# Kernel tuning notes

Hardware: AMD Instinct MI355X
Metric: run time of the kernel (lower is better)

Reference implementation:

```python
import jax, jax.numpy as jnp
import numpy as np

N_NODES = 20000
N_EDGES = 100000
WIDTH = 64
KER_IN = 6
KER_HID = WIDTH // 4  # 16
DEPTH = 6


def setup_inputs() -> dict:
    key = jax.random.key(0)
    ks = jax.random.split(key, 12)
    s = lambda fan_in: 1.0 / np.sqrt(fan_in)
    return {
        "x": jax.random.normal(ks[0], (N_NODES, 1), dtype=jnp.float32),
        "edge_index": jax.random.randint(ks[1], (2, N_EDGES), 0, N_NODES, dtype=jnp.int32),
        "edge_attr": jax.random.uniform(ks[2], (N_EDGES, KER_IN), dtype=jnp.float32),
        "fc1_w": jax.random.normal(ks[3], (1, WIDTH), dtype=jnp.float32) * s(1),
        "fc1_b": jnp.zeros((WIDTH,), dtype=jnp.float32),
        "k1_w": jax.random.normal(ks[4], (KER_IN, KER_HID), dtype=jnp.float32) * s(KER_IN),
        "k1_b": jnp.zeros((KER_HID,), dtype=jnp.float32),
        "k2_w": jax.random.normal(ks[5], (KER_HID, WIDTH * WIDTH), dtype=jnp.float32) * s(KER_HID),
        "k2_b": jnp.zeros((WIDTH * WIDTH,), dtype=jnp.float32),
        "root_w": jax.random.normal(ks[6], (WIDTH, WIDTH), dtype=jnp.float32) * s(WIDTH),
        "conv_b": jnp.zeros((WIDTH,), dtype=jnp.float32),
        "fc2_w": jax.random.normal(ks[7], (WIDTH, 1), dtype=jnp.float32) * s(WIDTH),
        "fc2_b": jnp.zeros((1,), dtype=jnp.float32),
    }


def reference(x, edge_index, edge_attr, fc1_w, fc1_b, k1_w, k1_b, k2_w, k2_b,
              root_w, conv_b, fc2_w, fc2_b):
    src = edge_index[0]  # source nodes j
    dst = edge_index[1]  # target nodes i

    # fc1: lift node features [N,1] -> [N,W]
    h = x @ fc1_w + fc1_b

    # Edge-conditioned weight matrices via kernel MLP (edge_attr is layer-invariant,
    # so compute once and reuse for all DEPTH layers — identical math).
    ek = jax.nn.relu(edge_attr @ k1_w + k1_b)           # [E, W/4]
    W = (ek @ k2_w + k2_b).reshape(N_EDGES, WIDTH, WIDTH)  # [E, W, W]

    # mean aggregation denominator (in-degree, clamped to avoid div-by-zero)
    deg = jax.ops.segment_sum(jnp.ones((N_EDGES,), dtype=h.dtype), dst,
                              num_segments=N_NODES)
    denom = jnp.maximum(deg, 1.0)[:, None]               # [N,1]

    for _ in range(DEPTH):
        # per-edge matmul: msg_e = x_src[e] @ W_e
        msg = jnp.einsum('ei,eio->eo', h[src], W)        # [E, W]
        agg = jax.ops.segment_sum(msg, dst, num_segments=N_NODES) / denom
        h = jax.nn.relu(agg + h @ root_w + conv_b)       # NNConv root weight + bias, then outer ReLU

    return h @ fc2_w + fc2_b                              # [N, 1]
```

## Files before the change

### kernel.cpp

```cpp
#include <hip/hip_runtime.h>
#include <hip/hip_bf16.h>


#define NN 20000
#define NE 100000
#define WD 64
#define DEPTH 6
#define TM 15
#define LSTR 1092

typedef __attribute__((ext_vector_type(8))) short bf16x8;
typedef __attribute__((ext_vector_type(4))) float f32x4;

__device__ __forceinline__ unsigned short f2bf(float v) {
    union { float f; unsigned u; } x; x.f = v;
    unsigned r = x.u + 0x7fffu + ((x.u >> 16) & 1u);
    return (unsigned short)(r >> 16);
}
__device__ __forceinline__ float bf2f(unsigned short b) {
    union { unsigned u; float f; } x; x.u = ((unsigned)b) << 16;
    return x.f;
}

__global__ __launch_bounds__(256) void count_kernel(const int* __restrict__ ei,
                                                    int* __restrict__ outc,
                                                    int* __restrict__ inc)
{
    int e = blockIdx.x * 256 + threadIdx.x;
    if (e >= NE) return;
    atomicAdd(&outc[ei[e]], 1);
    atomicAdd(&inc[ei[NE + e]], 1);
}

__global__ __launch_bounds__(256) void scanA_kernel(const int* __restrict__ cnt,
                                                    int* __restrict__ partials)
{
    int b = blockIdx.x, t = threadIdx.x, lane = t & 63, w = t >> 6;
    int base = b * 1024 + t * 4;
    int s = 0;
#pragma unroll
    for (int i = 0; i < 4; ++i) {
        int idx = base + i;
        if (idx < 2 * NN) s += cnt[idx];
    }
#pragma unroll
    for (int off = 32; off > 0; off >>= 1) s += __shfl_down(s, off, 64);
    __shared__ int wsum[4];
    if (lane == 0) wsum[w] = s;
    __syncthreads();
    if (t == 0) partials[b] = wsum[0] + wsum[1] + wsum[2] + wsum[3];
}

__global__ __launch_bounds__(64) void scanB_kernel(const int* __restrict__ partials,
                                                   int* __restrict__ bases)
{
    int l = threadIdx.x;
    int p = (l < 40) ? partials[l] : 0;
    int v = p;
#pragma unroll
    for (int off = 1; off < 64; off <<= 1) {
        int u = __shfl_up(v, off, 64);
        if (l >= off) v += u;
    }
    if (l < 40) bases[l] = v - p;
}

__global__ __launch_bounds__(256) void scanC_kernel(const int* __restrict__ cnt,
                                                    const int* __restrict__ bases,
                                                    int* __restrict__ rps,
                                                    int* __restrict__ rpd,
                                                    float* __restrict__ invd)
{
    int b = blockIdx.x, t = threadIdx.x, lane = t & 63, w = t >> 6;
    int base = b * 1024 + t * 4;
    int v[4], s = 0;
#pragma unroll
    for (int i = 0; i < 4; ++i) {
        int idx = base + i;
        v[i] = (idx < 2 * NN) ? cnt[idx] : 0;
        s += v[i];
    }
    int tsum = s, sc = s;
#pragma unroll
    for (int off = 1; off < 64; off <<= 1) {
        int u = __shfl_up(sc, off, 64);
        if (lane >= off) sc += u;
    }
    __shared__ int wtot[4];
    if (lane == 63) wtot[w] = sc;
    __syncthreads();
    int wbase = 0;
    for (int j = 0; j < w; ++j) wbase += wtot[j];
    int run = bases[b] + wbase + sc - tsum;
#pragma unroll
    for (int i = 0; i < 4; ++i) {
        int idx = base + i;
        int e = run; run += v[i];
        if (idx < NN) {
            rps[idx] = e;
        } else if (idx < 2 * NN) {
            rpd[idx - NN] = e - NE;
            invd[idx - NN] = 1.0f / fmaxf((float)v[i], 1.0f);
        }
    }
    if (b == 0 && t == 0) { rps[NN] = NE; rpd[NN] = NE; }
}

__global__ __launch_bounds__(256) void ekfill_kernel(
    const int* __restrict__ ei, const float* __restrict__ ea,
    const float* __restrict__ k1w, const float* __restrict__ k1b,
    const int* __restrict__ rps, const int* __restrict__ rpd,
    int* __restrict__ fs, int* __restrict__ fd,
    float* __restrict__ eks, int* __restrict__ ss2sd)
{
    int e = blockIdx.x * 256 + threadIdx.x;
    if (e >= NE) return;
    int s = ei[e], d = ei[NE + e];
    float a[6];
#pragma unroll
    for (int i = 0; i < 6; ++i) a[i] = ea[e * 6 + i];
    int slot_s = rps[s] + atomicAdd(&fs[s], 1);
    int slot_d = rpd[d] + atomicAdd(&fd[d], 1);
    ss2sd[slot_s] = slot_d;
#pragma unroll
    for (int j = 0; j < 16; ++j) {
        float v = k1b[j];
#pragma unroll
        for (int i = 0; i < 6; ++i) v = fmaf(a[i], k1w[i * 16 + j], v);
        eks[(size_t)slot_s * 16 + j] = fmaxf(v, 0.f);
    }
}

__global__ __launch_bounds__(256) void gwt_kernel(
    const float* __restrict__ k2w, const float* __restrict__ k2b,
    const float* __restrict__ rootw,
    unsigned short* __restrict__ Gh, unsigned short* __restrict__ Gl)
{
    int idx = blockIdx.x * 256 + threadIdx.x;
    if (idx >= 1152 * 64) return;
    int n = idx >> 6, k = idx & 63;
    int b = n >> 6, o = n & 63;
    float g;
    if (b < 16)       g = k2w[b * 4096 + k * 64 + o];
    else if (b == 16) g = k2b[k * 64 + o];
    else              g = rootw[k * 64 + o];
    unsigned short hi = f2bf(g);
    Gh[idx] = hi;
    Gl[idx] = f2bf(g - bf2f(hi));
}

__global__ __launch_bounds__(256) void h0_kernel(
    const float* __restrict__ x, const float* __restrict__ w,
    const float* __restrict__ b,
    unsigned short* __restrict__ hhi, unsigned short* __restrict__ hlo)
{
    int idx = blockIdx.x * 256 + threadIdx.x;
    if (idx >= NN * WD) return;
    int n = idx >> 6, o = idx & 63;
    float v = fmaf(x[n], w[o], b[o]);
    unsigned short hi = f2bf(v);
    hhi[idx] = hi;
    hlo[idx] = f2bf(v - bf2f(hi));
}

__global__ __launch_bounds__(512) void fused_kernel(
    const unsigned short* __restrict__ hhi, const unsigned short* __restrict__ hlo,
    const unsigned short* __restrict__ Gh, const unsigned short* __restrict__ Gl,
    const float* __restrict__ eks, const int* __restrict__ ss2sd,
    const int* __restrict__ rps, float* __restrict__ Proot,
    float* __restrict__ msg)
{
    __shared__ __align__(16) float Pt[TM * LSTR];
    __shared__ int rb[TM + 1];
    int n0 = blockIdx.x * TM;
    int w = threadIdx.x >> 6, l = threadIdx.x & 63;
    int quad = l >> 4, lr = l & 15;
    if (threadIdx.x < TM + 1) {
        int gi = n0 + threadIdx.x;
        rb[threadIdx.x] = rps[gi > NN ? NN : gi];
    }
    int arow = n0 + lr;
    if (arow > NN - 1) arow = NN - 1;
    const bf16x8* pah = (const bf16x8*)(hhi + (size_t)arow * 64 + quad * 8);
    const bf16x8* pal = (const bf16x8*)(hlo + (size_t)arow * 64 + quad * 8);
    bf16x8 ah0 = pah[0], ah1 = pah[4];
    bf16x8 al0 = pal[0], al1 = pal[4];

    for (int st = w; st < 18; st += 8) {
        f32x4 acc[4];
#pragma unroll
        for (int t = 0; t < 4; ++t) acc[t] = (f32x4){0.f, 0.f, 0.f, 0.f};
#pragma unroll
        for (int t = 0; t < 4; ++t) {
            int brow = st * 64 + t * 16 + lr;
            const bf16x8* pbh = (const bf16x8*)(Gh + (size_t)brow * 64 + quad * 8);
            const bf16x8* pbl = (const bf16x8*)(Gl + (size_t)brow * 64 + quad * 8);
            bf16x8 bh0 = pbh[0], bh1 = pbh[4];
            bf16x8 bl0 = pbl[0], bl1 = pbl[4];
            f32x4 a = acc[t];
            a = __builtin_amdgcn_mfma_f32_16x16x32_bf16(ah0, bh0, a, 0, 0, 0);
            a = __builtin_amdgcn_mfma_f32_16x16x32_bf16(ah0, bl0, a, 0, 0, 0);
            a = __builtin_amdgcn_mfma_f32_16x16x32_bf16(al0, bh0, a, 0, 0, 0);
            a = __builtin_amdgcn_mfma_f32_16x16x32_bf16(ah1, bh1, a, 0, 0, 0);
            a = __builtin_amdgcn_mfma_f32_16x16x32_bf16(ah1, bl1, a, 0, 0, 0);
            a = __builtin_amdgcn_mfma_f32_16x16x32_bf16(al1, bh1, a, 0, 0, 0);
            acc[t] = a;
        }
        if (st < 17) {
#pragma unroll
            for (int t = 0; t < 4; ++t)
#pragma unroll
                for (int r = 0; r < 4; ++r) {
                    int row = quad * 4 + r;
                    if (row < TM)
                        Pt[row * LSTR + st * 64 + t * 16 + lr] = acc[t][r];
                }
        } else {
#pragma unroll
            for (int t = 0; t < 4; ++t)
#pragma unroll
                for (int r = 0; r < 4; ++r) {
                    int row = quad * 4 + r;
                    int gn = n0 + row;
                    if (row < TM && gn < NN)
                        Proot[(size_t)gn * 64 + t * 16 + lr] = acc[t][r];
                }
        }
    }
    __syncthreads();

    int nend = n0 + TM; if (nend > NN) nend = NN;
    int r0 = rb[0], r1 = rb[nend - n0];
    int total = r1 - r0;
    if (total <= 0) return;
    int per = (total + 7) >> 3;
    int s0 = r0 + w * per;
    int s1 = s0 + per; if (s1 > r1) s1 = r1;
    int ln = 0;
    float p[17];
    bool need = true;
    for (int s = s0; s < s1; ++s) {
        while (s >= rb[ln + 1]) { ++ln; need = true; }
        if (need) {
            const float* Pr = &Pt[ln * LSTR];
#pragma unroll
            for (int k = 0; k < 17; ++k) p[k] = Pr[k * 64 + l];
            need = false;
        }
        int su = __builtin_amdgcn_readfirstlane(s);
        const float* er = eks + (size_t)su * 16;
        f32x4 e0 = *(const f32x4*)(er);
        f32x4 e1 = *(const f32x4*)(er + 4);
        f32x4 e2 = *(const f32x4*)(er + 8);
        f32x4 e3 = *(const f32x4*)(er + 12);
        int ds = ss2sd[su];
        float ma = p[16], mb = 0.f;
        ma = fmaf(e0[0], p[0], ma);  mb = fmaf(e0[1], p[1], mb);
        ma = fmaf(e0[2], p[2], ma);  mb = fmaf(e0[3], p[3], mb);
        ma = fmaf(e1[0], p[4], ma);  mb = fmaf(e1[1], p[5], mb);
        ma = fmaf(e1[2], p[6], ma);  mb = fmaf(e1[3], p[7], mb);
        ma = fmaf(e2[0], p[8], ma);  mb = fmaf(e2[1], p[9], mb);
        ma = fmaf(e2[2], p[10], ma); mb = fmaf(e2[3], p[11], mb);
        ma = fmaf(e3[0], p[12], ma); mb = fmaf(e3[1], p[13], mb);
        ma = fmaf(e3[2], p[14], ma); mb = fmaf(e3[3], p[15], mb);
        msg[(size_t)ds * 64 + l] = ma + mb;
    }
}

__global__ __launch_bounds__(256) void agg_kernel(
    const float* __restrict__ msg, const int* __restrict__ rpd,
    const float* __restrict__ invd, const float* __restrict__ Proot,
    const float* __restrict__ convb, float* __restrict__ h,
    unsigned short* __restrict__ hhi, unsigned short* __restrict__ hlo)
{
    int i = blockIdx.x * 4 + (threadIdx.x >> 6);
    if (i >= NN) return;
    int l = threadIdx.x & 63;
    int r0 = rpd[i], r1 = rpd[i + 1];
    float a0 = 0.f, a1 = 0.f, a2 = 0.f, a3 = 0.f;
    int s = r0;
    for (; s + 3 < r1; s += 4) {
        a0 += msg[(size_t)s * 64 + l];
        a1 += msg[(size_t)(s + 1) * 64 + l];
        a2 += msg[(size_t)(s + 2) * 64 + l];
        a3 += msg[(size_t)(s + 3) * 64 + l];
    }
    for (; s < r1; ++s) a0 += msg[(size_t)s * 64 + l];
    float acc = (a0 + a1) + (a2 + a3);
    float v = fmaf(acc, invd[i], Proot[(size_t)i * 64 + l] + convb[l]);
    v = fmaxf(v, 0.f);
    int idx = i * 64 + l;
    h[idx] = v;
    unsigned short hi = f2bf(v);
    hhi[idx] = hi;
    hlo[idx] = f2bf(v - bf2f(hi));
}

__global__ __launch_bounds__(256) void out_kernel(
    const float* __restrict__ h, const float* __restrict__ fc2_w,
    const float* __restrict__ fc2_b, float* __restrict__ out)
{
    int wave = blockIdx.x * 4 + (threadIdx.x >> 6);
    int lane = threadIdx.x & 63;
    float v = h[(size_t)wave * 64 + lane] * fc2_w[lane];
#pragma unroll
    for (int off = 32; off > 0; off >>= 1) v += __shfl_down(v, off);
    if (lane == 0) out[wave] = v + fc2_b[0];
}

extern "C" void kernel_launch(void* const* d_in, const int* in_sizes, int n_in,
                              void* d_out, int out_size, void* d_ws, size_t ws_size,
                              hipStream_t stream)
{
    const float* x         = (const float*)d_in[0];
    const int*   ei        = (const int*)  d_in[1];
    const float* edge_attr = (const float*)d_in[2];
    const float* fc1_w     = (const float*)d_in[3];
    const float* fc1_b     = (const float*)d_in[4];
    const float* k1_w      = (const float*)d_in[5];
    const float* k1_b      = (const float*)d_in[6];
    const float* k2_w      = (const float*)d_in[7];
    const float* k2_b      = (const float*)d_in[8];
    const float* root_w    = (const float*)d_in[9];
    const float* conv_b    = (const float*)d_in[10];
    const float* fc2_w     = (const float*)d_in[11];
    const float* fc2_b     = (const float*)d_in[12];
    float* out = (float*)d_out;

    float* ws = (float*)d_ws;
    size_t off = 0;
    int* cnt   = (int*)(ws + off); off += 4 * NN;
    int* outc  = cnt;
    int* inc   = cnt + NN;
    int* fs    = cnt + 2 * NN;
    int* fd    = cnt + 3 * NN;
    int* rps   = (int*)(ws + off); off += 20004;
    int* rpd   = (int*)(ws + off); off += 20004;
    int* partials = (int*)(ws + off); off += 64;
    int* bases    = (int*)(ws + off); off += 64;
    int* ss2sd    = (int*)(ws + off); off += NE;
    float* invd  = ws + off; off += NN;
    float* eks   = ws + off; off += (size_t)NE * 16;
    unsigned short* Gh  = (unsigned short*)(ws + off); off += 36864;
    unsigned short* Gl  = (unsigned short*)(ws + off); off += 36864;
    unsigned short* hhi = (unsigned short*)(ws + off); off += (size_t)NN * 32;
    unsigned short* hlo = (unsigned short*)(ws + off); off += (size_t)NN * 32;
    float* h     = ws + off; off += (size_t)NN * WD;
    float* msg   = ws + off; off += (size_t)NE * WD;
    float* Proot = ws + off; off += (size_t)NN * WD;

    hipMemsetAsync(cnt, 0, 4 * NN * sizeof(int), stream);
    count_kernel<<<(NE + 255) / 256, 256, 0, stream>>>(ei, outc, inc);
    scanA_kernel<<<40, 256, 0, stream>>>(cnt, partials);
    scanB_kernel<<<1, 64, 0, stream>>>(partials, bases);
    scanC_kernel<<<40, 256, 0, stream>>>(cnt, bases, rps, rpd, invd);
    ekfill_kernel<<<(NE + 255) / 256, 256, 0, stream>>>(ei, edge_attr, k1_w, k1_b,
                                                        rps, rpd, fs, fd, eks, ss2sd);
    gwt_kernel<<<(1152 * 64 + 255) / 256, 256, 0, stream>>>(k2_w, k2_b, root_w, Gh, Gl);
    h0_kernel<<<(NN * WD + 255) / 256, 256, 0, stream>>>(x, fc1_w, fc1_b, hhi, hlo);

    int ntiles = (NN + TM - 1) / TM;
    for (int layer = 0; layer < DEPTH; ++layer) {
        fused_kernel<<<ntiles, 512, 0, stream>>>(hhi, hlo, Gh, Gl, eks, ss2sd,
                                                 rps, Proot, msg);
        agg_kernel<<<(NN + 3) / 4, 256, 0, stream>>>(msg, rpd, invd, Proot,
                                                     conv_b, h, hhi, hlo);
    }

    out_kernel<<<NN / 4, 256, 0, stream>>>(h, fc2_w, fc2_b, out);
}
```

Before: 561.8 us.

## Aggregate per-destination edge features before the weight matmul, fusing layers into one kernel

The per-layer pipeline is reordered. Each destination node's incoming edges are first reduced into a 17x64 accumulator, z[k] = sum of ek[k]*h_src plus a plain h_src sum for the bias term, built in shared memory with LDS atomics. One bf16x3 MFMA against the transposed k2/k2b weights then produces the mean-aggregated message, and the root matmul, bias, ReLU and bf16 split are fused into the same kernel. This removes the per-edge msg buffer, the separate aggregation kernel and the source-side CSR, and ping-pongs the h buffers between layers. In exchange it adds a scalar gather of h rows per edge, LDS atomics, and a per-tile conversion of z to bf16 hi/lo pairs.

```diff
diff --git a/kernel.cpp b/kernel.cpp
--- a/kernel.cpp
+++ b/kernel.cpp
@@ -7,7 +7,7 @@
 #define WD 64
 #define DEPTH 6
 #define TM 15
-#define LSTR 1092
+#define ZSTR 1092
 
 typedef __attribute__((ext_vector_type(8))) short bf16x8;
 typedef __attribute__((ext_vector_type(4))) float f32x4;
@@ -23,12 +23,10 @@
 }
 
 __global__ __launch_bounds__(256) void count_kernel(const int* __restrict__ ei,
-                                                    int* __restrict__ outc,
                                                     int* __restrict__ inc)
 {
     int e = blockIdx.x * 256 + threadIdx.x;
     if (e >= NE) return;
-    atomicAdd(&outc[ei[e]], 1);
     atomicAdd(&inc[ei[NE + e]], 1);
 }
 
@@ -41,7 +39,7 @@
 #pragma unroll
     for (int i = 0; i < 4; ++i) {
         int idx = base + i;
-        if (idx < 2 * NN) s += cnt[idx];
+        if (idx < NN) s += cnt[idx];
     }
 #pragma unroll
     for (int off = 32; off > 0; off >>= 1) s += __shfl_down(s, off, 64);
@@ -55,19 +53,18 @@
                                                    int* __restrict__ bases)
 {
     int l = threadIdx.x;
-    int p = (l < 40) ? partials[l] : 0;
+    int p = (l < 20) ? partials[l] : 0;
     int v = p;
 #pragma unroll
     for (int off = 1; off < 64; off <<= 1) {
         int u = __shfl_up(v, off, 64);
         if (l >= off) v += u;
     }
-    if (l < 40) bases[l] = v - p;
+    if (l < 20) bases[l] = v - p;
 }
 
 __global__ __launch_bounds__(256) void scanC_kernel(const int* __restrict__ cnt,
                                                     const int* __restrict__ bases,
-                                                    int* __restrict__ rps,
                                                     int* __restrict__ rpd,
                                                     float* __restrict__ invd)
 {
@@ -77,7 +74,7 @@
 #pragma unroll
     for (int i = 0; i < 4; ++i) {
         int idx = base + i;
-        v[i] = (idx < 2 * NN) ? cnt[idx] : 0;
+        v[i] = (idx < NN) ? cnt[idx] : 0;
         s += v[i];
     }
     int tsum = s, sc = s;
@@ -97,21 +94,18 @@
         int idx = base + i;
         int e = run; run += v[i];
         if (idx < NN) {
-            rps[idx] = e;
-        } else if (idx < 2 * NN) {
-            rpd[idx - NN] = e - NE;
-            invd[idx - NN] = 1.0f / fmaxf((float)v[i], 1.0f);
-        }
-    }
-    if (b == 0 && t == 0) { rps[NN] = NE; rpd[NN] = NE; }
+            rpd[idx] = e;
+            invd[idx] = 1.0f / fmaxf((float)v[i], 1.0f);
+        }
+    }
+    if (b == 0 && t == 0) rpd[NN] = NE;
 }
 
 __global__ __launch_bounds__(256) void ekfill_kernel(
     const int* __restrict__ ei, const float* __restrict__ ea,
     const float* __restrict__ k1w, const float* __restrict__ k1b,
-    const int* __restrict__ rps, const int* __restrict__ rpd,
-    int* __restrict__ fs, int* __restrict__ fd,
-    float* __restrict__ eks, int* __restrict__ ss2sd)
+    const int* __restrict__ rpd, int* __restrict__ fd,
+    float* __restrict__ eks, int* __restrict__ srcs)
 {
     int e = blockIdx.x * 256 + threadIdx.x;
     if (e >= NE) return;
@@ -119,15 +113,14 @@
     float a[6];
 #pragma unroll
     for (int i = 0; i < 6; ++i) a[i] = ea[e * 6 + i];
-    int slot_s = rps[s] + atomicAdd(&fs[s], 1);
-    int slot_d = rpd[d] + atomicAdd(&fd[d], 1);
-    ss2sd[slot_s] = slot_d;
+    int slot = rpd[d] + atomicAdd(&fd[d], 1);
+    srcs[slot] = s;
 #pragma unroll
     for (int j = 0; j < 16; ++j) {
         float v = k1b[j];
 #pragma unroll
         for (int i = 0; i < 6; ++i) v = fmaf(a[i], k1w[i * 16 + j], v);
-        eks[(size_t)slot_s * 16 + j] = fmaxf(v, 0.f);
+        eks[(size_t)slot * 16 + j] = fmaxf(v, 0.f);
     }
 }
 
@@ -137,13 +130,12 @@
     unsigned short* __restrict__ Gh, unsigned short* __restrict__ Gl)
 {
     int idx = blockIdx.x * 256 + threadIdx.x;
-    if (idx >= 1152 * 64) return;
-    int n = idx >> 6, k = idx & 63;
-    int b = n >> 6, o = n & 63;
+    if (idx >= 64 * 1152) return;
+    int o = idx / 1152, c = idx % 1152;
     float g;
-    if (b < 16)       g = k2w[b * 4096 + k * 64 + o];
-    else if (b == 16) g = k2b[k * 64 + o];
-    else              g = rootw[k * 64 + o];
+    if (c < 1024)       g = k2w[(c >> 6) * 4096 + (c & 63) * 64 + o];
+    else if (c < 1088)  g = k2b[(c & 63) * 64 + o];
+    else                g = rootw[(c - 1088) * 64 + o];
     unsigned short hi = f2bf(g);
     Gh[idx] = hi;
     Gl[idx] = f2bf(g - bf2f(hi));
@@ -151,149 +143,161 @@
 
 __global__ __launch_bounds__(256) void h0_kernel(
     const float* __restrict__ x, const float* __restrict__ w,
-    const float* __restrict__ b,
+    const float* __restrict__ b, float* __restrict__ h,
     unsigned short* __restrict__ hhi, unsigned short* __restrict__ hlo)
 {
     int idx = blockIdx.x * 256 + threadIdx.x;
     if (idx >= NN * WD) return;
     int n = idx >> 6, o = idx & 63;
     float v = fmaf(x[n], w[o], b[o]);
-    unsigned short hi = f2bf(v);
-    hhi[idx] = hi;
-    hlo[idx] = f2bf(v - bf2f(hi));
-}
-
-__global__ __launch_bounds__(512) void fused_kernel(
-    const unsigned short* __restrict__ hhi, const unsigned short* __restrict__ hlo,
-    const unsigned short* __restrict__ Gh, const unsigned short* __restrict__ Gl,
-    const float* __restrict__ eks, const int* __restrict__ ss2sd,
-    const int* __restrict__ rps, float* __restrict__ Proot,
-    float* __restrict__ msg)
-{
-    __shared__ __align__(16) float Pt[TM * LSTR];
-    __shared__ int rb[TM + 1];
-    int n0 = blockIdx.x * TM;
-    int w = threadIdx.x >> 6, l = threadIdx.x & 63;
-    int quad = l >> 4, lr = l & 15;
-    if (threadIdx.x < TM + 1) {
-        int gi = n0 + threadIdx.x;
-        rb[threadIdx.x] = rps[gi > NN ? NN : gi];
-    }
-    int arow = n0 + lr;
-    if (arow > NN - 1) arow = NN - 1;
-    const bf16x8* pah = (const bf16x8*)(hhi + (size_t)arow * 64 + quad * 8);
-    const bf16x8* pal = (const bf16x8*)(hlo + (size_t)arow * 64 + quad * 8);
-    bf16x8 ah0 = pah[0], ah1 = pah[4];
-    bf16x8 al0 = pal[0], al1 = pal[4];
-
-    for (int st = w; st < 18; st += 8) {
-        f32x4 acc[4];
-#pragma unroll
-        for (int t = 0; t < 4; ++t) acc[t] = (f32x4){0.f, 0.f, 0.f, 0.f};
-#pragma unroll
-        for (int t = 0; t < 4; ++t) {
-            int brow = st * 64 + t * 16 + lr;
-            const bf16x8* pbh = (const bf16x8*)(Gh + (size_t)brow * 64 + quad * 8);
-            const bf16x8* pbl = (const bf16x8*)(Gl + (size_t)brow * 64 + quad * 8);
-            bf16x8 bh0 = pbh[0], bh1 = pbh[4];
-            bf16x8 bl0 = pbl[0], bl1 = pbl[4];
-            f32x4 a = acc[t];
-            a = __builtin_amdgcn_mfma_f32_16x16x32_bf16(ah0, bh0, a, 0, 0, 0);
-            a = __builtin_amdgcn_mfma_f32_16x16x32_bf16(ah0, bl0, a, 0, 0, 0);
-            a = __builtin_amdgcn_mfma_f32_16x16x32_bf16(al0, bh0, a, 0, 0, 0);
-            a = __builtin_amdgcn_mfma_f32_16x16x32_bf16(ah1, bh1, a, 0, 0, 0);
-            a = __builtin_amdgcn_mfma_f32_16x16x32_bf16(ah1, bl1, a, 0, 0, 0);
-            a = __builtin_amdgcn_mfma_f32_16x16x32_bf16(al1, bh1, a, 0, 0, 0);
-            acc[t] = a;
-        }
-        if (st < 17) {
-#pragma unroll
-            for (int t = 0; t < 4; ++t)
-#pragma unroll
-                for (int r = 0; r < 4; ++r) {
-                    int row = quad * 4 + r;
-                    if (row < TM)
-                        Pt[row * LSTR + st * 64 + t * 16 + lr] = acc[t][r];
-                }
-        } else {
-#pragma unroll
-            for (int t = 0; t < 4; ++t)
-#pragma unroll
-                for (int r = 0; r < 4; ++r) {
-                    int row = quad * 4 + r;
-                    int gn = n0 + row;
-                    if (row < TM && gn < NN)
-                        Proot[(size_t)gn * 64 + t * 16 + lr] = acc[t][r];
-                }
-        }
-    }
-    __syncthreads();
-
-    int nend = n0 + TM; if (nend > NN) nend = NN;
-    int r0 = rb[0], r1 = rb[nend - n0];
-    int total = r1 - r0;
-    if (total <= 0) return;
-    int per = (total + 7) >> 3;
-    int s0 = r0 + w * per;
-    int s1 = s0 + per; if (s1 > r1) s1 = r1;
-    int ln = 0;
-    float p[17];
-    bool need = true;
-    for (int s = s0; s < s1; ++s) {
-        while (s >= rb[ln + 1]) { ++ln; need = true; }
-        if (need) {
-            const float* Pr = &Pt[ln * LSTR];
-#pragma unroll
-            for (int k = 0; k < 17; ++k) p[k] = Pr[k * 64 + l];
-            need = false;
-        }
-        int su = __builtin_amdgcn_readfirstlane(s);
-        const float* er = eks + (size_t)su * 16;
-        f32x4 e0 = *(const f32x4*)(er);
-        f32x4 e1 = *(const f32x4*)(er + 4);
-        f32x4 e2 = *(const f32x4*)(er + 8);
-        f32x4 e3 = *(const f32x4*)(er + 12);
-        int ds = ss2sd[su];
-        float ma = p[16], mb = 0.f;
-        ma = fmaf(e0[0], p[0], ma);  mb = fmaf(e0[1], p[1], mb);
-        ma = fmaf(e0[2], p[2], ma);  mb = fmaf(e0[3], p[3], mb);
-        ma = fmaf(e1[0], p[4], ma);  mb = fmaf(e1[1], p[5], mb);
-        ma = fmaf(e1[2], p[6], ma);  mb = fmaf(e1[3], p[7], mb);
-        ma = fmaf(e2[0], p[8], ma);  mb = fmaf(e2[1], p[9], mb);
-        ma = fmaf(e2[2], p[10], ma); mb = fmaf(e2[3], p[11], mb);
-        ma = fmaf(e3[0], p[12], ma); mb = fmaf(e3[1], p[13], mb);
-        ma = fmaf(e3[2], p[14], ma); mb = fmaf(e3[3], p[15], mb);
-        msg[(size_t)ds * 64 + l] = ma + mb;
-    }
-}
-
-__global__ __launch_bounds__(256) void agg_kernel(
-    const float* __restrict__ msg, const int* __restrict__ rpd,
-    const float* __restrict__ invd, const float* __restrict__ Proot,
-    const float* __restrict__ convb, float* __restrict__ h,
-    unsigned short* __restrict__ hhi, unsigned short* __restrict__ hlo)
-{
-    int i = blockIdx.x * 4 + (threadIdx.x >> 6);
-    if (i >= NN) return;
-    int l = threadIdx.x & 63;
-    int r0 = rpd[i], r1 = rpd[i + 1];
-    float a0 = 0.f, a1 = 0.f, a2 = 0.f, a3 = 0.f;
-    int s = r0;
-    for (; s + 3 < r1; s += 4) {
-        a0 += msg[(size_t)s * 64 + l];
-        a1 += msg[(size_t)(s + 1) * 64 + l];
-        a2 += msg[(size_t)(s + 2) * 64 + l];
-        a3 += msg[(size_t)(s + 3) * 64 + l];
-    }
-    for (; s < r1; ++s) a0 += msg[(size_t)s * 64 + l];
-    float acc = (a0 + a1) + (a2 + a3);
-    float v = fmaf(acc, invd[i], Proot[(size_t)i * 64 + l] + convb[l]);
-    v = fmaxf(v, 0.f);
-    int idx = i * 64 + l;
     h[idx] = v;
     unsigned short hi = f2bf(v);
     hhi[idx] = hi;
     hlo[idx] = f2bf(v - bf2f(hi));
+}
+
+__global__ __launch_bounds__(512) void fused2_kernel(
+    const float* __restrict__ h, const unsigned short* __restrict__ hhi,
+    const unsigned short* __restrict__ hlo,
+    const unsigned short* __restrict__ Gh, const unsigned short* __restrict__ Gl,
+    const float* __restrict__ eks, const int* __restrict__ srcs,
+    const int* __restrict__ rpd, const float* __restrict__ invd,
+    const float* __restrict__ convb, float* __restrict__ hout,
+    unsigned short* __restrict__ hhio, unsigned short* __restrict__ hloo)
+{
+    __shared__ __align__(16) float Zt[TM * ZSTR];
+    __shared__ int rb[TM + 1];
+    int n0 = blockIdx.x * TM;
+    int tid = threadIdx.x;
+    int w = tid >> 6, l = tid & 63;
+    int quad = l >> 4, lr = l & 15;
+    if (tid < TM + 1) {
+        int gi = n0 + tid;
+        rb[tid] = rpd[gi > NN ? NN : gi];
+    }
+    for (int i = tid; i < TM * ZSTR; i += 512) Zt[i] = 0.f;
+    __syncthreads();
+
+    int nend = n0 + TM; if (nend > NN) nend = NN;
+    int tmeff = nend - n0;
+    int r0 = rb[0], r1 = rb[tmeff];
+    int total = r1 - r0;
+    if (total > 0) {
+        int per = (total + 7) >> 3;
+        int s0 = r0 + w * per;
+        int s1 = s0 + per; if (s1 > r1) s1 = r1;
+        if (s0 < s1) {
+            int ln = 0;
+            while (s0 >= rb[ln + 1]) ++ln;
+            float z[17];
+#pragma unroll
+            for (int k = 0; k < 17; ++k) z[k] = 0.f;
+            bool dirty = false;
+            for (int s = s0; s < s1; ++s) {
+                if (s >= rb[ln + 1]) {
+                    if (dirty) {
+#pragma unroll
+                        for (int k = 0; k < 17; ++k)
+                            atomicAdd(&Zt[ln * ZSTR + k * 64 + l], z[k]);
+#pragma unroll
+                        for (int k = 0; k < 17; ++k) z[k] = 0.f;
+                        dirty = false;
+                    }
+                    while (s >= rb[ln + 1]) ++ln;
+                }
+                int su = __builtin_amdgcn_readfirstlane(s);
+                int sn = srcs[su];
+                float hv = h[(size_t)sn * 64 + l];
+                const float* er = eks + (size_t)su * 16;
+                f32x4 e0 = *(const f32x4*)(er);
+                f32x4 e1 = *(const f32x4*)(er + 4);
+                f32x4 e2 = *(const f32x4*)(er + 8);
+                f32x4 e3 = *(const f32x4*)(er + 12);
+                z[0]  = fmaf(e0[0], hv, z[0]);   z[1]  = fmaf(e0[1], hv, z[1]);
+                z[2]  = fmaf(e0[2], hv, z[2]);   z[3]  = fmaf(e0[3], hv, z[3]);
+                z[4]  = fmaf(e1[0], hv, z[4]);   z[5]  = fmaf(e1[1], hv, z[5]);
+                z[6]  = fmaf(e1[2], hv, z[6]);   z[7]  = fmaf(e1[3], hv, z[7]);
+                z[8]  = fmaf(e2[0], hv, z[8]);   z[9]  = fmaf(e2[1], hv, z[9]);
+                z[10] = fmaf(e2[2], hv, z[10]);  z[11] = fmaf(e2[3], hv, z[11]);
+                z[12] = fmaf(e3[0], hv, z[12]);  z[13] = fmaf(e3[1], hv, z[13]);
+                z[14] = fmaf(e3[2], hv, z[14]);  z[15] = fmaf(e3[3], hv, z[15]);
+                z[16] += hv;
+                dirty = true;
+            }
+            if (dirty) {
+#pragma unroll
+                for (int k = 0; k < 17; ++k)
+                    atomicAdd(&Zt[ln * ZSTR + k * 64 + l], z[k]);
+            }
+        }
+    }
+    __syncthreads();
+
+    int st = w & 3, kh = w >> 2;
+    int brow = st * 16 + lr;
+    int rowA = (lr < tmeff) ? lr : 0;
+    f32x4 acc = (f32x4){0.f, 0.f, 0.f, 0.f};
+    for (int ks = kh * 17; ks < kh * 17 + 17; ++ks) {
+        const f32x4* pz = (const f32x4*)&Zt[rowA * ZSTR + ks * 32 + quad * 8];
+        f32x4 z0 = pz[0], z1 = pz[1];
+        bf16x8 ah, al;
+#pragma unroll
+        for (int j = 0; j < 4; ++j) {
+            unsigned short hi0 = f2bf(z0[j]);
+            ah[j] = (short)hi0; al[j] = (short)f2bf(z0[j] - bf2f(hi0));
+            unsigned short hi1 = f2bf(z1[j]);
+            ah[4 + j] = (short)hi1; al[4 + j] = (short)f2bf(z1[j] - bf2f(hi1));
+        }
+        const bf16x8* pbh = (const bf16x8*)(Gh + (size_t)brow * 1152 + ks * 32 + quad * 8);
+        const bf16x8* pbl = (const bf16x8*)(Gl + (size_t)brow * 1152 + ks * 32 + quad * 8);
+        bf16x8 bh = pbh[0], bl = pbl[0];
+        acc = __builtin_amdgcn_mfma_f32_16x16x32_bf16(ah, bh, acc, 0, 0, 0);
+        acc = __builtin_amdgcn_mfma_f32_16x16x32_bf16(ah, bl, acc, 0, 0, 0);
+        acc = __builtin_amdgcn_mfma_f32_16x16x32_bf16(al, bh, acc, 0, 0, 0);
+    }
+    f32x4 accR = (f32x4){0.f, 0.f, 0.f, 0.f};
+    if (kh == 1) {
+        int arow = n0 + lr;
+        if (arow > NN - 1) arow = NN - 1;
+#pragma unroll
+        for (int ks2 = 0; ks2 < 2; ++ks2) {
+            const bf16x8* pah = (const bf16x8*)(hhi + (size_t)arow * 64 + ks2 * 32 + quad * 8);
+            const bf16x8* pal = (const bf16x8*)(hlo + (size_t)arow * 64 + ks2 * 32 + quad * 8);
+            bf16x8 ah = pah[0], al = pal[0];
+            const bf16x8* pbh = (const bf16x8*)(Gh + (size_t)brow * 1152 + 1088 + ks2 * 32 + quad * 8);
+            const bf16x8* pbl = (const bf16x8*)(Gl + (size_t)brow * 1152 + 1088 + ks2 * 32 + quad * 8);
+            bf16x8 bh = pbh[0], bl = pbl[0];
+            accR = __builtin_amdgcn_mfma_f32_16x16x32_bf16(ah, bh, accR, 0, 0, 0);
+            accR = __builtin_amdgcn_mfma_f32_16x16x32_bf16(ah, bl, accR, 0, 0, 0);
+            accR = __builtin_amdgcn_mfma_f32_16x16x32_bf16(al, bh, accR, 0, 0, 0);
+        }
+    }
+    __syncthreads();
+    if (kh == 0) {
+#pragma unroll
+        for (int r = 0; r < 4; ++r)
+            Zt[st * 256 + (quad * 4 + r) * 16 + lr] = acc[r];
+    }
+    __syncthreads();
+    if (kh == 1) {
+        int col = st * 16 + lr;
+        float cb = convb[col];
+#pragma unroll
+        for (int r = 0; r < 4; ++r) {
+            int row = quad * 4 + r;
+            int gn = n0 + row;
+            if (row < tmeff) {
+                float aggv = acc[r] + Zt[st * 256 + row * 16 + lr];
+                float v = fmaf(aggv, invd[gn], accR[r] + cb);
+                v = fmaxf(v, 0.f);
+                size_t idx = (size_t)gn * 64 + col;
+                hout[idx] = v;
+                unsigned short hi = f2bf(v);
+                hhio[idx] = hi;
+                hloo[idx] = f2bf(v - bf2f(hi));
+            }
+        }
+    }
 }
 
 __global__ __launch_bounds__(256) void out_kernel(
@@ -329,43 +333,45 @@
 
     float* ws = (float*)d_ws;
     size_t off = 0;
-    int* cnt   = (int*)(ws + off); off += 4 * NN;
-    int* outc  = cnt;
-    int* inc   = cnt + NN;
-    int* fs    = cnt + 2 * NN;
-    int* fd    = cnt + 3 * NN;
-    int* rps   = (int*)(ws + off); off += 20004;
+    int* cnt   = (int*)(ws + off); off += 2 * NN;
+    int* inc   = cnt;
+    int* fd    = cnt + NN;
     int* rpd   = (int*)(ws + off); off += 20004;
     int* partials = (int*)(ws + off); off += 64;
     int* bases    = (int*)(ws + off); off += 64;
-    int* ss2sd    = (int*)(ws + off); off += NE;
+    int* srcs  = (int*)(ws + off); off += NE;
     float* invd  = ws + off; off += NN;
     float* eks   = ws + off; off += (size_t)NE * 16;
     unsigned short* Gh  = (unsigned short*)(ws + off); off += 36864;
     unsigned short* Gl  = (unsigned short*)(ws + off); off += 36864;
-    unsigned short* hhi = (unsigned short*)(ws + off); off += (size_t)NN * 32;
-    unsigned short* hlo = (unsigned short*)(ws + off); off += (size_t)NN * 32;
-    float* h     = ws + off; off += (size_t)NN * WD;
-    float* msg   = ws + off; off += (size_t)NE * WD;
-    float* Proot = ws + off; off += (size_t)NN * WD;
-
-    hipMemsetAsync(cnt, 0, 4 * NN * sizeof(int), stream);
-    count_kernel<<<(NE + 255) / 256, 256, 0, stream>>>(ei, outc, inc);
-    scanA_kernel<<<40, 256, 0, stream>>>(cnt, partials);
+    unsigned short* hhiA = (unsigned short*)(ws + off); off += (size_t)NN * 32;
+    unsigned short* hloA = (unsigned short*)(ws + off); off += (size_t)NN * 32;
+    unsigned short* hhiB = (unsigned short*)(ws + off); off += (size_t)NN * 32;
+    unsigned short* hloB = (unsigned short*)(ws + off); off += (size_t)NN * 32;
+    float* hA    = ws + off; off += (size_t)NN * WD;
+    float* hB    = ws + off; off += (size_t)NN * WD;
+
+    hipMemsetAsync(cnt, 0, 2 * NN * sizeof(int), stream);
+    count_kernel<<<(NE + 255) / 256, 256, 0, stream>>>(ei, inc);
+    scanA_kernel<<<20, 256, 0, stream>>>(inc, partials);
     scanB_kernel<<<1, 64, 0, stream>>>(partials, bases);
-    scanC_kernel<<<40, 256, 0, stream>>>(cnt, bases, rps, rpd, invd);
+    scanC_kernel<<<20, 256, 0, stream>>>(inc, bases, rpd, invd);
     ekfill_kernel<<<(NE + 255) / 256, 256, 0, stream>>>(ei, edge_attr, k1_w, k1_b,
-                                                        rps, rpd, fs, fd, eks, ss2sd);
-    gwt_kernel<<<(1152 * 64 + 255) / 256, 256, 0, stream>>>(k2_w, k2_b, root_w, Gh, Gl);
-    h0_kernel<<<(NN * WD + 255) / 256, 256, 0, stream>>>(x, fc1_w, fc1_b, hhi, hlo);
+                                                        rpd, fd, eks, srcs);
+    gwt_kernel<<<(64 * 1152 + 255) / 256, 256, 0, stream>>>(k2_w, k2_b, root_w, Gh, Gl);
+    h0_kernel<<<(NN * WD + 255) / 256, 256, 0, stream>>>(x, fc1_w, fc1_b, hA, hhiA, hloA);
 
     int ntiles = (NN + TM - 1) / TM;
+    float* hin = hA;  unsigned short* hhi_i = hhiA; unsigned short* hlo_i = hloA;
+    float* hto = hB;  unsigned short* hhi_o = hhiB; unsigned short* hlo_o = hloB;
     for (int layer = 0; layer < DEPTH; ++layer) {
-        fused_kernel<<<ntiles, 512, 0, stream>>>(hhi, hlo, Gh, Gl, eks, ss2sd,
-                                                 rps, Proot, msg);
-        agg_kernel<<<(NN + 3) / 4, 256, 0, stream>>>(msg, rpd, invd, Proot,
-                                                     conv_b, h, hhi, hlo);
-    }
-
-    out_kernel<<<NN / 4, 256, 0, stream>>>(h, fc2_w, fc2_b, out);
-}
+        fused2_kernel<<<ntiles, 512, 0, stream>>>(hin, hhi_i, hlo_i, Gh, Gl,
+                                                  eks, srcs, rpd, invd, conv_b,
+                                                  hto, hhi_o, hlo_o);
+        float* tf = hin; hin = hto; hto = tf;
+        unsigned short* t1 = hhi_i; hhi_i = hhi_o; hhi_o = t1;
+        unsigned short* t2 = hlo_i; hlo_i = hlo_o; hlo_o = t2;
+    }
+
+    out_kernel<<<NN / 4, 256, 0, stream>>>(hin, fc2_w, fc2_b, out);
+}
```

After: 1.350 ms. +140.3%, slower.

## Shrink node tile to 8, bound occupancy, restructure per-node edge loop

Applied to the files above, without the earlier changes.

Reduces nodes per block from 15 to 8, which halves the LDS tile and doubles the grid size. It also asks the compiler to fit 8 blocks per CU through launch bounds. The MFMA loop now computes and stores one 16-column tile at a time instead of holding four accumulators, and the edge loop iterates per node over clipped ranges instead of scanning row boundaries inside the edge loop. The aim is lower register and LDS pressure for more occupancy. The cost is that half the MFMA rows are wasted, since 16-row tiles now carry only 8 nodes, and the shared-weight B operand is reloaded by twice as many blocks.

```diff
diff --git a/kernel.cpp b/kernel.cpp
--- a/kernel.cpp
+++ b/kernel.cpp
@@ -6,7 +6,7 @@
 #define NE 100000
 #define WD 64
 #define DEPTH 6
-#define TM 15
+#define TM 8
 #define LSTR 1092
 
 typedef __attribute__((ext_vector_type(8))) short bf16x8;
@@ -163,7 +163,7 @@
     hlo[idx] = f2bf(v - bf2f(hi));
 }
 
-__global__ __launch_bounds__(512) void fused_kernel(
+__global__ __launch_bounds__(512, 8) void fused_kernel(
     const unsigned short* __restrict__ hhi, const unsigned short* __restrict__ hlo,
     const unsigned short* __restrict__ Gh, const unsigned short* __restrict__ Gl,
     const float* __restrict__ eks, const int* __restrict__ ss2sd,
@@ -187,83 +187,81 @@
     bf16x8 al0 = pal[0], al1 = pal[4];
 
     for (int st = w; st < 18; st += 8) {
-        f32x4 acc[4];
-#pragma unroll
-        for (int t = 0; t < 4; ++t) acc[t] = (f32x4){0.f, 0.f, 0.f, 0.f};
 #pragma unroll
         for (int t = 0; t < 4; ++t) {
             int brow = st * 64 + t * 16 + lr;
-            const bf16x8* pbh = (const bf16x8*)(Gh + (size_t)brow * 64 + quad * 8);
-            const bf16x8* pbl = (const bf16x8*)(Gl + (size_t)brow * 64 + quad * 8);
-            bf16x8 bh0 = pbh[0], bh1 = pbh[4];
-            bf16x8 bl0 = pbl[0], bl1 = pbl[4];
-            f32x4 a = acc[t];
-            a = __builtin_amdgcn_mfma_f32_16x16x32_bf16(ah0, bh0, a, 0, 0, 0);
-            a = __builtin_amdgcn_mfma_f32_16x16x32_bf16(ah0, bl0, a, 0, 0, 0);
-            a = __builtin_amdgcn_mfma_f32_16x16x32_bf16(al0, bh0, a, 0, 0, 0);
-            a = __builtin_amdgcn_mfma_f32_16x16x32_bf16(ah1, bh1, a, 0, 0, 0);
-            a = __builtin_amdgcn_mfma_f32_16x16x32_bf16(ah1, bl1, a, 0, 0, 0);
-            a = __builtin_amdgcn_mfma_f32_16x16x32_bf16(al1, bh1, a, 0, 0, 0);
-            acc[t] = a;
-        }
-        if (st < 17) {
-#pragma unroll
-            for (int t = 0; t < 4; ++t)
+            f32x4 a = (f32x4){0.f, 0.f, 0.f, 0.f};
+            {
+                const bf16x8* pbh = (const bf16x8*)(Gh + (size_t)brow * 64 + quad * 8);
+                const bf16x8* pbl = (const bf16x8*)(Gl + (size_t)brow * 64 + quad * 8);
+                bf16x8 bh0 = pbh[0], bl0 = pbl[0];
+                a = __builtin_amdgcn_mfma_f32_16x16x32_bf16(ah0, bh0, a, 0, 0, 0);
+                a = __builtin_amdgcn_mfma_f32_16x16x32_bf16(ah0, bl0, a, 0, 0, 0);
+                a = __builtin_amdgcn_mfma_f32_16x16x32_bf16(al0, bh0, a, 0, 0, 0);
+            }
+            {
+                const bf16x8* pbh = (const bf16x8*)(Gh + (size_t)brow * 64 + 32 + quad * 8);
+                const bf16x8* pbl = (const bf16x8*)(Gl + (size_t)brow * 64 + 32 + quad * 8);
+                bf16x8 bh1 = pbh[0], bl1 = pbl[0];
+                a = __builtin_amdgcn_mfma_f32_16x16x32_bf16(ah1, bh1, a, 0, 0, 0);
+                a = __builtin_amdgcn_mfma_f32_16x16x32_bf16(ah1, bl1, a, 0, 0, 0);
+                a = __builtin_amdgcn_mfma_f32_16x16x32_bf16(al1, bh1, a, 0, 0, 0);
+            }
+            if (st < 17) {
 #pragma unroll
                 for (int r = 0; r < 4; ++r) {
                     int row = quad * 4 + r;
                     if (row < TM)
-                        Pt[row * LSTR + st * 64 + t * 16 + lr] = acc[t][r];
+                        Pt[row * LSTR + st * 64 + t * 16 + lr] = a[r];
                 }
-        } else {
-#pragma unroll
-            for (int t = 0; t < 4; ++t)
+            } else {
 #pragma unroll
                 for (int r = 0; r < 4; ++r) {
                     int row = quad * 4 + r;
                     int gn = n0 + row;
                     if (row < TM && gn < NN)
-                        Proot[(size_t)gn * 64 + t * 16 + lr] = acc[t][r];
+                        Proot[(size_t)gn * 64 + t * 16 + lr] = a[r];
                 }
+            }
         }
     }
     __syncthreads();
 
     int nend = n0 + TM; if (nend > NN) nend = NN;
-    int r0 = rb[0], r1 = rb[nend - n0];
+    int tmeff = nend - n0;
+    int r0 = rb[0], r1 = rb[tmeff];
     int total = r1 - r0;
     if (total <= 0) return;
     int per = (total + 7) >> 3;
     int s0 = r0 + w * per;
     int s1 = s0 + per; if (s1 > r1) s1 = r1;
-    int ln = 0;
-    float p[17];
-    bool need = true;
-    for (int s = s0; s < s1; ++s) {
-        while (s >= rb[ln + 1]) { ++ln; need = true; }
-        if (need) {
-            const float* Pr = &Pt[ln * LSTR];
-#pragma unroll
-            for (int k = 0; k < 17; ++k) p[k] = Pr[k * 64 + l];
-            need = false;
+    for (int ln = 0; ln < tmeff && s0 < s1; ++ln) {
+        int lo = s0 > rb[ln] ? s0 : rb[ln];
+        int hi = s1 < rb[ln + 1] ? s1 : rb[ln + 1];
+        if (lo >= hi) continue;
+        float p[17];
+        const float* Pr = &Pt[ln * LSTR];
+#pragma unroll
+        for (int k = 0; k < 17; ++k) p[k] = Pr[k * 64 + l];
+        for (int s = lo; s < hi; ++s) {
+            int su = __builtin_amdgcn_readfirstlane(s);
+            const float* er = eks + (size_t)su * 16;
+            f32x4 e0 = *(const f32x4*)(er);
+            f32x4 e1 = *(const f32x4*)(er + 4);
+            f32x4 e2 = *(const f32x4*)(er + 8);
+            f32x4 e3 = *(const f32x4*)(er + 12);
+            int ds = ss2sd[su];
+            float ma = p[16], mb = 0.f;
+            ma = fmaf(e0[0], p[0], ma);  mb = fmaf(e0[1], p[1], mb);
+            ma = fmaf(e0[2], p[2], ma);  mb = fmaf(e0[3], p[3], mb);
+            ma = fmaf(e1[0], p[4], ma);  mb = fmaf(e1[1], p[5], mb);
+            ma = fmaf(e1[2], p[6], ma);  mb = fmaf(e1[3], p[7], mb);
+            ma = fmaf(e2[0], p[8], ma);  mb = fmaf(e2[1], p[9], mb);
+            ma = fmaf(e2[2], p[10], ma); mb = fmaf(e2[3], p[11], mb);
+            ma = fmaf(e3[0], p[12], ma); mb = fmaf(e3[1], p[13], mb);
+            ma = fmaf(e3[2], p[14], ma); mb = fmaf(e3[3], p[15], mb);
+            msg[(size_t)ds * 64 + l] = ma + mb;
         }
-        int su = __builtin_amdgcn_readfirstlane(s);
-        const float* er = eks + (size_t)su * 16;
-        f32x4 e0 = *(const f32x4*)(er);
-        f32x4 e1 = *(const f32x4*)(er + 4);
-        f32x4 e2 = *(const f32x4*)(er + 8);
-        f32x4 e3 = *(const f32x4*)(er + 12);
-        int ds = ss2sd[su];
-        float ma = p[16], mb = 0.f;
-        ma = fmaf(e0[0], p[0], ma);  mb = fmaf(e0[1], p[1], mb);
-        ma = fmaf(e0[2], p[2], ma);  mb = fmaf(e0[3], p[3], mb);
-        ma = fmaf(e1[0], p[4], ma);  mb = fmaf(e1[1], p[5], mb);
-        ma = fmaf(e1[2], p[6], ma);  mb = fmaf(e1[3], p[7], mb);
-        ma = fmaf(e2[0], p[8], ma);  mb = fmaf(e2[1], p[9], mb);
-        ma = fmaf(e2[2], p[10], ma); mb = fmaf(e2[3], p[11], mb);
-        ma = fmaf(e3[0], p[12], ma); mb = fmaf(e3[1], p[13], mb);
-        ma = fmaf(e3[2], p[14], ma); mb = fmaf(e3[3], p[15], mb);
-        msg[(size_t)ds * 64 + l] = ma + mb;
     }
 }
 
```

Measured after the change: 749.9 us. 1.33x slower.
